# Optimization experiments

Hardware: AMD Instinct MI355X
Metric: run time of the kernel (lower is better)

The kernel has to match this reference:

```python
import jax, jax.numpy as jnp
import numpy as np

D_MODEL = 1024
NUM_HEADS = 16


def setup_inputs() -> dict:
    key = jax.random.key(0)
    ks = jax.random.split(key, 5)
    B, S, D = 4, 2048, D_MODEL
    std = (2.0 / (D + D)) ** 0.5
    x = jax.random.normal(ks[0], (B, S, D), dtype=jnp.float32)
    Wq = jax.random.normal(ks[1], (D, D), dtype=jnp.float32) * std
    Wk = jax.random.normal(ks[2], (D, D), dtype=jnp.float32) * std
    Wv = jax.random.normal(ks[3], (D, D), dtype=jnp.float32) * std
    Wo = jax.random.normal(ks[4], (D, D), dtype=jnp.float32) * std
    return {"x": x, "Wq": Wq, "Wk": Wk, "Wv": Wv, "Wo": Wo}


def reference(x, Wq, Wk, Wv, Wo):
    # x: [B, S, D]; W*: [out, in] applied as einsum('od,...d->...o')
    B, S, D = x.shape
    H = NUM_HEADS
    dk = D // H

    def split_heads(t):  # [B, S, D] -> [B, H, S, dk]
        return t.reshape(B, S, H, dk).transpose(0, 2, 1, 3)

    q = split_heads(jnp.einsum('od,bsd->bso', Wq, x))
    k = split_heads(jnp.einsum('od,bsd->bso', Wk, x))
    v = split_heads(jnp.einsum('od,bsd->bso', Wv, x))

    # materialized scores: [B, H, S, S]
    scores = jnp.einsum('bhqd,bhkd->bhqk', q, k) / jnp.sqrt(jnp.asarray(dk, x.dtype))
    causal = jnp.tril(jnp.ones((S, S), dtype=bool))  # query attends to keys <= query
    scores = jnp.where(causal, scores, -jnp.inf)
    attn = jax.nn.softmax(scores, axis=-1)
    out = jnp.einsum('bhqk,bhkd->bhqd', attn, v)  # [B, H, S, dk]
    out = out.transpose(0, 2, 1, 3).reshape(B, S, D)
    return jnp.einsum('od,bsd->bso', Wo, out)
```

## Files before the change

### kernel.cpp

```cpp
#include <hip/hip_runtime.h>
#include <math.h>

#define SEQ  2048
#define NBH  64
#define QT_N (SEQ/128)

typedef __bf16 bf16;
typedef float  f4v   __attribute__((ext_vector_type(4)));
typedef float  f32x4 __attribute__((ext_vector_type(4)));
typedef __bf16 bf16x8 __attribute__((ext_vector_type(8)));
typedef __bf16 bf16x4 __attribute__((ext_vector_type(4)));

typedef unsigned int u32g __attribute__((address_space(1)));
typedef unsigned int u32l __attribute__((address_space(3)));

__device__ __forceinline__ void async16(const void* g, void* l) {
    __builtin_amdgcn_global_load_lds((const u32g*)g, (u32l*)l, 16, 0, 0);
}

__global__ __launch_bounds__(256)
void castall(const float* __restrict__ x,  const float* __restrict__ wq,
             const float* __restrict__ wk, const float* __restrict__ wv,
             const float* __restrict__ wo, bf16* __restrict__ dst)
{
    const int i = (blockIdx.x * 256 + threadIdx.x) * 4;
    const float* s; int off; float sc = 1.f;
    if (i < 8388608)       { s = x;  off = 0; }
    else if (i < 9437184)  { s = wq; off = 8388608;  sc = 0.18033688011f; }
    else if (i < 10485760) { s = wk; off = 9437184;  }
    else if (i < 11534336) { s = wv; off = 10485760; }
    else                   { s = wo; off = 11534336; }
    f4v v = *(const f4v*)&s[i - off];
    bf16x4 o;
    o[0] = (bf16)(v[0] * sc);
    o[1] = (bf16)(v[1] * sc);
    o[2] = (bf16)(v[2] * sc);
    o[3] = (bf16)(v[3] * sc);
    *(bf16x4*)&dst[i] = o;
}

template<int MODE>
__global__ __launch_bounds__(256)
void gemm_bf16(const bf16* __restrict__ A, const bf16* __restrict__ Bw,
               bf16* __restrict__ Oq, bf16* __restrict__ Ok, bf16* __restrict__ Ov,
               float* __restrict__ Of)
{
    __shared__ bf16 As[4096];
    __shared__ bf16 Bs[4096];

    const int t    = threadIdx.x;
    const int lane = t & 63;
    const int w    = t >> 6;
    const int m0   = blockIdx.y * 128;
    const int n0   = blockIdx.x * 128;
    const int wr   = (w >> 1) * 64;
    const int wc   = (w & 1) * 64;
    const int lr   = lane & 15;
    const int lk   = lane >> 4;

    f32x4 acc[4][4];
    #pragma unroll
    for (int i = 0; i < 4; ++i)
        #pragma unroll
        for (int j = 0; j < 4; ++j) acc[i][j] = f32x4{0.f, 0.f, 0.f, 0.f};

    int rowi[2], srcoff[2];
    #pragma unroll
    for (int it = 0; it < 2; ++it) {
        int b    = t * 16 + it * 4096;
        int row  = b >> 6;
        int koff = b & 63;
        rowi[it]   = row;
        srcoff[it] = (koff ^ (((row >> 1) & 3) << 4)) >> 1;
    }
    const bf16* Abase = A  + (size_t)m0 * 1024;
    const bf16* Bbase = Bw + (size_t)n0 * 1024;

    for (int k0 = 0; k0 < 1024; k0 += 32) {
        __syncthreads();
        #pragma unroll
        for (int it = 0; it < 2; ++it) {
            async16(Abase + (size_t)rowi[it] * 1024 + k0 + srcoff[it],
                    &As[w * 512 + it * 2048]);
            async16(Bbase + (size_t)rowi[it] * 1024 + k0 + srcoff[it],
                    &Bs[w * 512 + it * 2048]);
        }
        __syncthreads();

        bf16x8 af[4], bfr[4];
        #pragma unroll
        for (int mi = 0; mi < 4; ++mi) {
            int row = wr + mi * 16 + lr;
            af[mi] = *(const bf16x8*)((const char*)As + row * 64 +
                                      ((lk * 16) ^ (((row >> 1) & 3) << 4)));
        }
        #pragma unroll
        for (int ni = 0; ni < 4; ++ni) {
            int row = wc + ni * 16 + lr;
            bfr[ni] = *(const bf16x8*)((const char*)Bs + row * 64 +
                                       ((lk * 16) ^ (((row >> 1) & 3) << 4)));
        }
        #pragma unroll
        for (int mi = 0; mi < 4; ++mi)
            #pragma unroll
            for (int ni = 0; ni < 4; ++ni)
                acc[mi][ni] = __builtin_amdgcn_mfma_f32_16x16x32_bf16(
                    af[mi], bfr[ni], acc[mi][ni], 0, 0, 0);
    }

    #pragma unroll
    for (int mi = 0; mi < 4; ++mi) {
        #pragma unroll
        for (int r = 0; r < 4; ++r) {
            int m = m0 + wr + mi * 16 + lk * 4 + r;
            if (MODE == 0) {
                int bb = m >> 11, ss = m & 2047;
                #pragma unroll
                for (int ni = 0; ni < 4; ++ni) {
                    int n   = n0 + wc + ni * 16 + lr;
                    int mat = n >> 10;
                    int o   = n & 1023;
                    int hh  = o >> 6, dd = o & 63;
                    bf16* dst = (mat == 0) ? Oq : (mat == 1) ? Ok : Ov;
                    dst[(((size_t)(bb * 16 + hh)) * SEQ + ss) * 64 + dd] =
                        (bf16)acc[mi][ni][r];
                }
            } else {
                #pragma unroll
                for (int ni = 0; ni < 4; ++ni) {
                    int n = n0 + wc + ni * 16 + lr;
                    Of[(size_t)m * 1024 + n] = acc[mi][ni][r];
                }
            }
        }
    }
}

__global__ __launch_bounds__(256)
void vtrans(const bf16* __restrict__ V, bf16* __restrict__ Vt) {
    __shared__ bf16 ts[64][72];
    const int bh = blockIdx.y;
    const int st = blockIdx.x;
    const int t  = threadIdx.x;
    const int r  = t >> 3;
    const int c8 = (t & 7) * 8;

    #pragma unroll
    for (int it = 0; it < 2; ++it) {
        int row = r + it * 32;
        bf16x8 v = *(const bf16x8*)&V[((size_t)bh * SEQ + st * 64 + row) * 64 + c8];
        #pragma unroll
        for (int j = 0; j < 8; ++j) ts[c8 + j][row] = v[j];
    }
    __syncthreads();
    #pragma unroll
    for (int it = 0; it < 2; ++it) {
        int dk = r + it * 32;
        bf16x8 v = *(const bf16x8*)&ts[dk][c8];
        *(bf16x8*)&Vt[((size_t)bh * 64 + dk) * SEQ + st * 64 + c8] = v;
    }
}

__global__ __launch_bounds__(512)
void fattn(const bf16* __restrict__ Q, const bf16* __restrict__ K,
           const bf16* __restrict__ Vt, bf16* __restrict__ AO)
{
    __shared__ bf16 Ks[2][4096];
    __shared__ bf16 Vs[2][4096];
    __shared__ bf16 Ps[8][1024];

    const int pr   = blockIdx.x;
    const int bh   = blockIdx.y;
    const int t    = threadIdx.x;
    const int lane = t & 63;
    const int w    = t >> 6;
    const int lr   = lane & 15;
    const int lk   = lane >> 4;
    const int b    = bh >> 4, h = bh & 15;

    const int by   = t * 16;
    const int srow = by >> 7;
    const int soff = ((by & 127) ^ ((srow & 7) << 4)) >> 1;

    #pragma unroll 1
    for (int seg = 0; seg < 2; ++seg) {
        const int qt  = seg ? pr : (QT_N - 1 - pr);
        const int q0  = qt * 128 + w * 16;
        const int nkv = 2 * qt + 2;

        bf16x8 qf[2];
        #pragma unroll
        for (int kc = 0; kc < 2; ++kc)
            qf[kc] = *(const bf16x8*)
                &Q[((size_t)bh * SEQ + q0 + lr) * 64 + kc * 32 + lk * 8];

        f32x4 oacc[4];
        float l_[4];
        #pragma unroll
        for (int r = 0; r < 4; ++r) l_[r] = 0.f;
        #pragma unroll
        for (int nd = 0; nd < 4; ++nd) oacc[nd] = f32x4{0.f, 0.f, 0.f, 0.f};

        async16(&K [((size_t)bh * SEQ + srow) * 64 + soff], &Ks[0][w * 512]);
        async16(&Vt[((size_t)bh * 64 + srow) * SEQ + soff], &Vs[0][w * 512]);

        for (int kv = 0; kv < nkv; ++kv) {
            const int cur = kv & 1;
            if (kv + 1 < nkv) {
                const int nxt = cur ^ 1;
                async16(&K [((size_t)bh * SEQ + (kv + 1) * 64 + srow) * 64 + soff],
                        &Ks[nxt][w * 512]);
                async16(&Vt[((size_t)bh * 64 + srow) * SEQ + (kv + 1) * 64 + soff],
                        &Vs[nxt][w * 512]);
                asm volatile("s_waitcnt vmcnt(2)" ::: "memory");
            } else {
                asm volatile("s_waitcnt vmcnt(0)" ::: "memory");
            }
            __builtin_amdgcn_s_barrier();

            if (kv * 64 <= q0 + 15) {
                f32x4 sv[4];
                #pragma unroll
                for (int ni = 0; ni < 4; ++ni) sv[ni] = f32x4{0.f,0.f,0.f,0.f};
                __builtin_amdgcn_s_setprio(1);
                #pragma unroll
                for (int ni = 0; ni < 4; ++ni) {
                    #pragma unroll
                    for (int kc = 0; kc < 2; ++kc) {
                        int krow = ni * 16 + lr;
                        bf16x8 kf = *(const bf16x8*)((const char*)&Ks[cur][0] + krow * 128 +
                                    ((kc * 64 + lk * 16) ^ ((krow & 7) << 4)));
                        sv[ni] = __builtin_amdgcn_mfma_f32_16x16x32_bf16(
                            qf[kc], kf, sv[ni], 0, 0, 0);
                    }
                }
                __builtin_amdgcn_s_setprio(0);
                if (kv * 64 + 63 > q0) {
                    #pragma unroll
                    for (int ni = 0; ni < 4; ++ni)
                        #pragma unroll
                        for (int r = 0; r < 4; ++r) {
                            int qg = q0 + lk * 4 + r;
                            int kp = kv * 64 + ni * 16 + lr;
                            if (kp > qg) sv[ni][r] = -3.0e38f;
                        }
                }
                #pragma unroll
                for (int r = 0; r < 4; ++r) {
                    int   prow  = lk * 4 + r;
                    char* pbase = (char*)&Ps[w][0] + prow * 128;
                    #pragma unroll
                    for (int ni = 0; ni < 4; ++ni) {
                        float p = exp2f(sv[ni][r]);
                        l_[r] += p;
                        int col2 = (ni * 16 + lr) * 2;
                        *(bf16*)(pbase + (col2 ^ ((prow & 7) << 4))) = (bf16)p;
                    }
                }
                __builtin_amdgcn_s_setprio(1);
                #pragma unroll
                for (int kc = 0; kc < 2; ++kc) {
                    bf16x8 pa = *(const bf16x8*)((const char*)&Ps[w][0] + lr * 128 +
                                ((kc * 64 + lk * 16) ^ ((lr & 7) << 4)));
                    #pragma unroll
                    for (int nd = 0; nd < 4; ++nd) {
                        int vrow = nd * 16 + lr;
                        bf16x8 vf = *(const bf16x8*)((const char*)&Vs[cur][0] + vrow * 128 +
                                    ((kc * 64 + lk * 16) ^ ((vrow & 7) << 4)));
                        oacc[nd] = __builtin_amdgcn_mfma_f32_16x16x32_bf16(
                            pa, vf, oacc[nd], 0, 0, 0);
                    }
                }
                __builtin_amdgcn_s_setprio(0);
            }
            __builtin_amdgcn_s_barrier();
        }

        #pragma unroll
        for (int r = 0; r < 4; ++r) {
            #pragma unroll
            for (int off = 1; off < 16; off <<= 1)
                l_[r] += __shfl_xor(l_[r], off);
        }
        #pragma unroll
        for (int r = 0; r < 4; ++r) {
            int   srow2 = q0 + lk * 4 + r;
            float rl    = 1.f / l_[r];
            #pragma unroll
            for (int nd = 0; nd < 4; ++nd) {
                int dk = nd * 16 + lr;
                AO[((size_t)(b * SEQ + srow2)) * 1024 + h * 64 + dk] =
                    (bf16)(oacc[nd][r] * rl);
            }
        }
    }
}

extern "C" void kernel_launch(void* const* d_in, const int* in_sizes, int n_in,
                              void* d_out, int out_size, void* d_ws, size_t ws_size,
                              hipStream_t stream)
{
    const float* x  = (const float*)d_in[0];
    const float* Wq = (const float*)d_in[1];
    const float* Wk = (const float*)d_in[2];
    const float* Wv = (const float*)d_in[3];
    const float* Wo = (const float*)d_in[4];
    float* out = (float*)d_out;

    const size_t NE = (size_t)8192 * 1024;
    bf16* Xb    = (bf16*)d_ws;
    bf16* Wqkvb = Xb + NE;
    bf16* Wob   = Wqkvb + (size_t)3 * 1024 * 1024;
    bf16* Qb    = Wob   + (size_t)1024 * 1024;
    bf16* Kb    = Qb  + NE;
    bf16* Vb    = Kb  + NE;
    bf16* Vtb   = Vb  + NE;
    bf16* AOb   = Vtb + NE;

    castall<<<12288, 256, 0, stream>>>(x, Wq, Wk, Wv, Wo, Xb);

    dim3 g1(24, 64);
    gemm_bf16<0><<<g1, 256, 0, stream>>>(Xb, Wqkvb, Qb, Kb, Vb, nullptr);

    vtrans<<<dim3(32, 64), 256, 0, stream>>>(Vb, Vtb);

    fattn<<<dim3(8, NBH), 512, 0, stream>>>(Qb, Kb, Vtb, AOb);

    dim3 g3(8, 64);
    gemm_bf16<1><<<g3, 256, 0, stream>>>(AOb, Wob, nullptr, nullptr, nullptr, out);
}
```

Before: 266.4 us.

## Replace QKV projection GEMM with 256x256-tile, 8-wave double-buffered kernel

Adds a new QKV projection kernel that uses 256x256 output tiles across 8 waves, with double-buffered async global-to-LDS loads, swizzled LDS reads, and MFMA phases interleaved with barriers and setprio. The larger tile cuts the global and LDS traffic per FLOP and overlaps the next K tile's loads with compute. In exchange it needs 128KB of dynamic shared memory, which limits occupancy, and launches only 384 blocks, which may leave some CUs underused. It also adds a hipFuncSetAttribute call on every launch.

New measurement: 270.4 us. Within noise of the previous version (+1.5%).

```diff
diff --git a/kernel.cpp b/kernel.cpp
--- a/kernel.cpp
+++ b/kernel.cpp
@@ -39,6 +39,153 @@
     *(bf16x4*)&dst[i] = o;
 }
 
+__global__ __launch_bounds__(512, 2)
+void gemm8(const bf16* __restrict__ A, const bf16* __restrict__ Bw,
+           bf16* __restrict__ Oq, bf16* __restrict__ Ok, bf16* __restrict__ Ov)
+{
+    extern __shared__ bf16 lds[];
+    const int t    = threadIdx.x;
+    const int lane = t & 63;
+    const int w    = t >> 6;
+    const int lr   = lane & 15;
+    const int lk   = lane >> 4;
+    const int m0   = blockIdx.y * 256;
+    const int n0   = blockIdx.x * 256;
+    const int wr   = (w >> 2) * 128;
+    const int wc   = (w & 3) * 64;
+
+    const int swz = (lr & 7) << 4;
+    const int ko0 = (lk * 16) ^ swz;
+    const int ko1 = (64 + lk * 16) ^ swz;
+
+    const int srow0 = t >> 3;
+    const int soff0 = (((t * 16) & 127) ^ ((srow0 & 7) << 4)) >> 1;
+    const bf16* Ag = A  + (size_t)(m0 + srow0) * 1024 + soff0;
+    const bf16* Bg = Bw + (size_t)(n0 + srow0) * 1024 + soff0;
+
+    f32x4 acc[8][4];
+    #pragma unroll
+    for (int mi = 0; mi < 8; ++mi)
+        #pragma unroll
+        for (int ni = 0; ni < 4; ++ni) acc[mi][ni] = f32x4{0.f, 0.f, 0.f, 0.f};
+
+    auto STAGE = [&](int kt, int bsel) {
+        bf16* Ad = lds + bsel * 32768 + w * 512;
+        bf16* Bd = Ad + 16384;
+        #pragma unroll
+        for (int j = 0; j < 4; ++j)
+            async16(Ag + (size_t)j * 65536 + kt * 64, Ad + j * 4096);
+        #pragma unroll
+        for (int j = 0; j < 4; ++j)
+            async16(Bg + (size_t)j * 65536 + kt * 64, Bd + j * 4096);
+    };
+
+#define ARD(buf, R, KO) (*(const bf16x8*)((const char*)(buf) + (R) * 128 + (KO)))
+#define MFMA_(a, b, c) __builtin_amdgcn_mfma_f32_16x16x32_bf16(a, b, c, 0, 0, 0)
+
+    STAGE(0, 0);
+    asm volatile("s_waitcnt vmcnt(0)" ::: "memory");
+    __builtin_amdgcn_s_barrier();
+
+    for (int tt = 0; tt < 16; ++tt) {
+        const int cur = tt & 1;
+        const bf16* Ab = lds + cur * 32768;
+        const bf16* Bb = Ab + 16384;
+        if (tt + 1 < 16) STAGE(tt + 1, cur ^ 1);
+
+        bf16x8 av[4][2], blo[2][2], bhi[2][2];
+        #pragma unroll
+        for (int mi = 0; mi < 4; ++mi) {
+            int R = wr + mi * 16 + lr;
+            av[mi][0] = ARD(Ab, R, ko0);
+            av[mi][1] = ARD(Ab, R, ko1);
+        }
+        #pragma unroll
+        for (int ni = 0; ni < 2; ++ni) {
+            int R = wc + ni * 16 + lr;
+            blo[ni][0] = ARD(Bb, R, ko0);
+            blo[ni][1] = ARD(Bb, R, ko1);
+        }
+        __builtin_amdgcn_s_barrier();
+        __builtin_amdgcn_s_setprio(1);
+        #pragma unroll
+        for (int mi = 0; mi < 4; ++mi)
+            #pragma unroll
+            for (int ni = 0; ni < 2; ++ni)
+                #pragma unroll
+                for (int kk = 0; kk < 2; ++kk)
+                    acc[mi][ni] = MFMA_(av[mi][kk], blo[ni][kk], acc[mi][ni]);
+        __builtin_amdgcn_s_setprio(0);
+        __builtin_amdgcn_s_barrier();
+        #pragma unroll
+        for (int ni = 0; ni < 2; ++ni) {
+            int R = wc + (ni + 2) * 16 + lr;
+            bhi[ni][0] = ARD(Bb, R, ko0);
+            bhi[ni][1] = ARD(Bb, R, ko1);
+        }
+        __builtin_amdgcn_s_barrier();
+        __builtin_amdgcn_s_setprio(1);
+        #pragma unroll
+        for (int mi = 0; mi < 4; ++mi)
+            #pragma unroll
+            for (int ni = 0; ni < 2; ++ni)
+                #pragma unroll
+                for (int kk = 0; kk < 2; ++kk)
+                    acc[mi][ni + 2] = MFMA_(av[mi][kk], bhi[ni][kk], acc[mi][ni + 2]);
+        __builtin_amdgcn_s_setprio(0);
+        __builtin_amdgcn_s_barrier();
+        #pragma unroll
+        for (int mi = 0; mi < 4; ++mi) {
+            int R = wr + (mi + 4) * 16 + lr;
+            av[mi][0] = ARD(Ab, R, ko0);
+            av[mi][1] = ARD(Ab, R, ko1);
+        }
+        __builtin_amdgcn_s_barrier();
+        __builtin_amdgcn_s_setprio(1);
+        #pragma unroll
+        for (int mi = 0; mi < 4; ++mi)
+            #pragma unroll
+            for (int ni = 0; ni < 2; ++ni)
+                #pragma unroll
+                for (int kk = 0; kk < 2; ++kk)
+                    acc[mi + 4][ni + 2] = MFMA_(av[mi][kk], bhi[ni][kk], acc[mi + 4][ni + 2]);
+        __builtin_amdgcn_s_setprio(0);
+        __builtin_amdgcn_s_barrier();
+        __builtin_amdgcn_s_setprio(1);
+        #pragma unroll
+        for (int mi = 0; mi < 4; ++mi)
+            #pragma unroll
+            for (int ni = 0; ni < 2; ++ni)
+                #pragma unroll
+                for (int kk = 0; kk < 2; ++kk)
+                    acc[mi + 4][ni] = MFMA_(av[mi][kk], blo[ni][kk], acc[mi + 4][ni]);
+        __builtin_amdgcn_s_setprio(0);
+        if (tt + 1 < 16) asm volatile("s_waitcnt vmcnt(0)" ::: "memory");
+        __builtin_amdgcn_s_barrier();
+    }
+
+    #pragma unroll
+    for (int mi = 0; mi < 8; ++mi) {
+        #pragma unroll
+        for (int rr = 0; rr < 4; ++rr) {
+            int m  = m0 + wr + mi * 16 + lk * 4 + rr;
+            int bb = m >> 11, ss = m & 2047;
+            #pragma unroll
+            for (int ni = 0; ni < 4; ++ni) {
+                int n   = n0 + wc + ni * 16 + lr;
+                int mat = n >> 10;
+                int o   = n & 1023;
+                int hh  = o >> 6, dd = o & 63;
+                bf16* dst = (mat == 0) ? Oq : (mat == 1) ? Ok : Ov;
+                dst[(((size_t)(bb * 16 + hh)) * SEQ + ss) * 64 + dd] =
+                    (bf16)acc[mi][ni][rr];
+            }
+        }
+    }
+#undef ARD
+#undef MFMA_
+}
+
 template<int MODE>
 __global__ __launch_bounds__(256)
 void gemm_bf16(const bf16* __restrict__ A, const bf16* __restrict__ Bw,
@@ -317,10 +464,12 @@
     bf16* Vtb   = Vb  + NE;
     bf16* AOb   = Vtb + NE;
 
+    hipFuncSetAttribute(reinterpret_cast<const void*>(&gemm8),
+                        hipFuncAttributeMaxDynamicSharedMemorySize, 131072);
+
     castall<<<12288, 256, 0, stream>>>(x, Wq, Wk, Wv, Wo, Xb);
 
-    dim3 g1(24, 64);
-    gemm_bf16<0><<<g1, 256, 0, stream>>>(Xb, Wqkvb, Qb, Kb, Vb, nullptr);
+    gemm8<<<dim3(12, 32), 512, 131072, stream>>>(Xb, Wqkvb, Qb, Kb, Vb);
 
     vtrans<<<dim3(32, 64), 256, 0, stream>>>(Vb, Vtb);
 
```
